# Optimization experiments

Hardware: AMD Instinct MI355X
Metric: run time of the kernel (lower is better)

Reference implementation:

```python
import jax, jax.numpy as jnp
import numpy as np

N_NODES = 50000
N_EDGES = 800000
IN_DIM = 64
HID = 128
OUT_DIM = 64
T_HIST = 8


def setup_inputs() -> dict:
    key = jax.random.key(0)
    ks = jax.random.split(key, 12)
    s = 0.05
    return {
        "node_feats": jax.random.normal(ks[0], (N_NODES, IN_DIM), jnp.float32),
        "history_feats": jax.random.normal(ks[1], (N_NODES, T_HIST, HID), jnp.float32),
        "src": jax.random.randint(ks[2], (N_EDGES,), 0, N_NODES, jnp.int32),
        "dst": jax.random.randint(ks[3], (N_EDGES,), 0, N_NODES, jnp.int32),
        # SAGEConv params (fc_self, fc_neigh share bias as in DGL)
        "W_self": jax.random.normal(ks[4], (IN_DIM, HID), jnp.float32) * s,
        "W_neigh": jax.random.normal(ks[5], (IN_DIM, HID), jnp.float32) * s,
        "b_sage": jnp.zeros((HID,), jnp.float32),
        # LSTM params, PyTorch gate order [i, f, g, o]
        "w_ih": jax.random.normal(ks[6], (HID, 4 * HID), jnp.float32) * s,
        "w_hh": jax.random.normal(ks[7], (HID, 4 * HID), jnp.float32) * s,
        "b_lstm": jnp.zeros((4 * HID,), jnp.float32),
        # classifier
        "W_cls": jax.random.normal(ks[8], (HID, OUT_DIM), jnp.float32) * s,
        "b_cls": jnp.zeros((OUT_DIM,), jnp.float32),
    }


def _lstm_last(x, w_ih, w_hh, b):
    # x: [N, T, H] -> last hidden state [N, H]
    N, T, H = x.shape

    def step(carry, xt):
        h, c = carry
        gates = xt @ w_ih + h @ w_hh + b  # [N, 4H]
        i, f, g, o = jnp.split(gates, 4, axis=-1)
        c = jax.nn.sigmoid(f) * c + jax.nn.sigmoid(i) * jnp.tanh(g)
        h = jax.nn.sigmoid(o) * jnp.tanh(c)
        return (h, c), None

    h0 = jnp.zeros((N, H), x.dtype)
    (h, _), _ = jax.lax.scan(step, (h0, h0), jnp.swapaxes(x, 0, 1))
    return h


def reference(node_feats, history_feats, src, dst, W_self, W_neigh, b_sage,
              w_ih, w_hh, b_lstm, W_cls, b_cls):
    N = node_feats.shape[0]
    # SAGEConv mean aggregation: mean of in-neighbor features per dst node
    msg_sum = jax.ops.segment_sum(node_feats[src], dst, num_segments=N)
    deg = jax.ops.segment_sum(jnp.ones((src.shape[0],), node_feats.dtype),
                              dst, num_segments=N)
    h_neigh = msg_sum / jnp.maximum(deg, 1.0)[:, None]
    h_struct = node_feats @ W_self + h_neigh @ W_neigh + b_sage  # [N, HID]
    # LSTM over history, take last timestep
    h_temp = _lstm_last(history_feats, w_ih, w_hh, b_lstm)  # [N, HID]
    h_combined = h_struct + h_temp
    return h_combined @ W_cls + b_cls  # [N, OUT_DIM]
```

## Files before the change

kernel.cpp:

```cpp
#include <hip/hip_runtime.h>
#include <hip/hip_bf16.h>
#include <stdint.h>

#define N_NODES 50000
#define N_EDGES 800000
#define IN_DIM 64
#define HID 128
#define OUT_DIM 64
#define T_HIST 8

#define NB_SCAN ((N_NODES + 1023) / 1024)

typedef __attribute__((ext_vector_type(8))) short short8;
typedef __attribute__((ext_vector_type(4))) float f32x4;

__device__ __forceinline__ unsigned short f2bf(float x) {
  unsigned int u = __builtin_bit_cast(unsigned int, x);
  unsigned int r = (u + 0x7FFFu + ((u >> 16) & 1u)) >> 16;
  return (unsigned short)r;
}
__device__ __forceinline__ short8 cvt8(float4 a, float4 b) {
  unsigned int w0, w1, w2, w3;
  asm("v_cvt_pk_bf16_f32 %0, %1, %2" : "=v"(w0) : "v"(a.x), "v"(a.y));
  asm("v_cvt_pk_bf16_f32 %0, %1, %2" : "=v"(w1) : "v"(a.z), "v"(a.w));
  asm("v_cvt_pk_bf16_f32 %0, %1, %2" : "=v"(w2) : "v"(b.x), "v"(b.y));
  asm("v_cvt_pk_bf16_f32 %0, %1, %2" : "=v"(w3) : "v"(b.z), "v"(b.w));
  struct { unsigned int a, b, c, d; } s{w0, w1, w2, w3};
  return __builtin_bit_cast(short8, s);
}
__device__ __forceinline__ float sigm(float x) {
  float e = __builtin_amdgcn_exp2f(-1.4426950408889634f * x);
  return __builtin_amdgcn_rcpf(1.f + e);
}
__device__ __forceinline__ float tanh_f(float x) {
  float e = __builtin_amdgcn_exp2f(2.8853900817779268f * x);
  return 1.f - 2.f * __builtin_amdgcn_rcpf(e + 1.f);
}

__global__ void pc_kernel(const float* __restrict__ w_ih, const float* __restrict__ w_hh,
                          const float* __restrict__ W_cls,
                          const float* __restrict__ W_self, const float* __restrict__ W_neigh,
                          const float* __restrict__ b_sage, const float* __restrict__ b_cls,
                          const int* __restrict__ dst,
                          unsigned short* __restrict__ Wt2, unsigned short* __restrict__ Wc2,
                          float* __restrict__ Wsc, float* __restrict__ Wnc,
                          float* __restrict__ bc1, int* __restrict__ cnt) {
  int tid = blockIdx.x * blockDim.x + threadIdx.x;
  int stride = gridDim.x * blockDim.x;
  for (int e = tid; e < N_EDGES; e += stride) atomicAdd(&cnt[dst[e]], 1);
  for (int idx = tid; idx < 256 * 512; idx += stride) {
    int i = idx & 7;
    int lane = (idx >> 3) & 63;
    int F = idx >> 9;
    int q = F >> 5, g = (F >> 3) & 3, kk = F & 7;
    int c = g * 128 + q * 16 + (lane & 15);
    int k = kk * 32 + (lane >> 4) * 8 + i;
    float v = (k < 128) ? w_ih[k * 512 + c] : w_hh[(k - 128) * 512 + c];
    Wt2[idx] = f2bf(v);
  }
  for (int idx = tid; idx < 16 * 512; idx += stride) {
    int i = idx & 7;
    int lane = (idx >> 3) & 63;
    int F = idx >> 9;
    int cb = F >> 2, kk = F & 3;
    int col = cb * 16 + (lane & 15);
    int k = kk * 32 + (lane >> 4) * 8 + i;
    Wc2[idx] = f2bf(W_cls[k * 64 + col]);
  }
  for (int idx = tid; idx < 64 * 64; idx += stride) {
    int k = idx >> 6, c = idx & 63;
    float as = 0.f, an = 0.f;
    for (int m = 0; m < 128; m++) {
      float wc = W_cls[m * 64 + c];
      as += W_self[k * 128 + m] * wc;
      an += W_neigh[k * 128 + m] * wc;
    }
    Wsc[idx] = as;
    Wnc[idx] = an;
  }
  for (int c = tid; c < 64; c += stride) {
    float acc = b_cls[c];
    for (int m = 0; m < 128; m++) acc += b_sage[m] * W_cls[m * 64 + c];
    bc1[c] = acc;
  }
}

__global__ __launch_bounds__(256) void scan1_kernel(const int* __restrict__ cnt,
                                                    int* __restrict__ lexcl, int* __restrict__ btot) {
  __shared__ int sh[256];
  int tid = threadIdx.x;
  int base = blockIdx.x * 1024 + tid * 4;
  int v[4];
  #pragma unroll
  for (int q = 0; q < 4; q++) {
    int i = base + q;
    v[q] = (i < N_NODES) ? cnt[i] : 0;
  }
  int tsum = v[0] + v[1] + v[2] + v[3];
  sh[tid] = tsum;
  __syncthreads();
  int val = tsum;
  for (int off = 1; off < 256; off <<= 1) {
    int x = (tid >= off) ? sh[tid - off] : 0;
    __syncthreads();
    val += x;
    sh[tid] = val;
    __syncthreads();
  }
  int ex = val - tsum;
  if (tid == 255) btot[blockIdx.x] = val;
  #pragma unroll
  for (int q = 0; q < 4; q++) {
    int i = base + q;
    if (i < N_NODES) lexcl[i] = ex;
    ex += v[q];
  }
}

__global__ __launch_bounds__(1024) void scan3_kernel(const int* __restrict__ lexcl,
                                                     const int* __restrict__ btot,
                                                     int* __restrict__ rowstart, int* __restrict__ cursor) {
  int b = blockIdx.x;
  int bs = 0;
  for (int j = 0; j < b; j++) bs += btot[j];
  int i = b * 1024 + threadIdx.x;
  if (i < N_NODES) {
    int rs = lexcl[i] + bs;
    rowstart[i] = rs;
    cursor[i] = rs;
  }
}

__global__ void fill_kernel(const int* __restrict__ src, const int* __restrict__ dst,
                            int* __restrict__ cursor, int* __restrict__ esrc) {
  int e = blockIdx.x * blockDim.x + threadIdx.x;
  if (e < N_EDGES) {
    int d = dst[e];
    int pos = atomicAdd(&cursor[d], 1);
    esrc[pos] = src[e];
  }
}

#define HS_TILE 32
__global__ __launch_bounds__(512) void hstruct_kernel(
    const float* __restrict__ nf, const int* __restrict__ esrc,
    const int* __restrict__ rowstart, const int* __restrict__ cnt,
    const float* __restrict__ Wsc, const float* __restrict__ Wnc, const float* __restrict__ bc1,
    float* __restrict__ out1) {
  __shared__ float s_nf[HS_TILE][IN_DIM + 1];
  __shared__ float s_hn[HS_TILE][IN_DIM + 1];
  int tid = threadIdx.x;
  int node0 = blockIdx.x * HS_TILE;
  for (int i = tid; i < HS_TILE * IN_DIM; i += 512) {
    int r = i >> 6, k = i & 63;
    int node = node0 + r;
    s_nf[r][k] = (node < N_NODES) ? nf[node * 64 + k] : 0.f;
  }
  int wv = tid >> 6, lane = tid & 63;
  for (int r = wv; r < HS_TILE; r += 8) {
    int node = node0 + r;
    float a0 = 0.f, a1 = 0.f, a2 = 0.f, a3 = 0.f;
    int n = 0;
    if (node < N_NODES) {
      n = cnt[node];
      int st = rowstart[node];
      int j = 0;
      for (; j + 4 <= n; j += 4) {
        int s0 = esrc[st + j], s1 = esrc[st + j + 1];
        int s2 = esrc[st + j + 2], s3 = esrc[st + j + 3];
        a0 += nf[s0 * 64 + lane];
        a1 += nf[s1 * 64 + lane];
        a2 += nf[s2 * 64 + lane];
        a3 += nf[s3 * 64 + lane];
      }
      for (; j < n; j++) a0 += nf[esrc[st + j] * 64 + lane];
    }
    s_hn[r][lane] = (a0 + a1 + a2 + a3) * __builtin_amdgcn_rcpf(fmaxf((float)n, 1.f));
  }
  __syncthreads();
  int r = tid & 31;
  int c0 = (tid >> 5) * 4;
  float accs[4] = {0.f, 0.f, 0.f, 0.f};
  for (int k = 0; k < IN_DIM; k++) {
    float a = s_nf[r][k];
    float b = s_hn[r][k];
    float4 w1 = *(const float4*)&Wsc[k * 64 + c0];
    float4 w2 = *(const float4*)&Wnc[k * 64 + c0];
    accs[0] += a * w1.x + b * w2.x;
    accs[1] += a * w1.y + b * w2.y;
    accs[2] += a * w1.z + b * w2.z;
    accs[3] += a * w1.w + b * w2.w;
  }
  int node = node0 + r;
  if (node < N_NODES) {
    #pragma unroll
    for (int i = 0; i < 4; i++)
      out1[(size_t)node * 64 + c0 + i] = accs[i] + bc1[c0 + i];
  }
}

#define LB 32
__global__ __launch_bounds__(512, 2) void lstm_kernel(
    const float* __restrict__ hist,
    const unsigned short* __restrict__ Wt2,
    const unsigned short* __restrict__ Wc2,
    const float* __restrict__ b_lstm,
    const float* __restrict__ out1,
    float* __restrict__ out)
{
  __shared__ alignas(16) unsigned short Abuf[2][LB * 256];

  const int tid = threadIdx.x;
  const int lane = tid & 63;
  const int w = tid >> 6;
  const int l15 = lane & 15;
  const int l4 = lane >> 4;
  const int base = blockIdx.x * LB;
  const int jj = w * 16 + l15;

  short8 Bfr[4][8];
  #pragma unroll
  for (int g = 0; g < 4; g++)
    #pragma unroll
    for (int kk = 0; kk < 8; kk++)
      Bfr[g][kk] = *(const short8*)&Wt2[((w * 32 + g * 8 + kk) * 64 + lane) * 8];

  const float bi  = b_lstm[jj];
  const float bf_ = b_lstm[128 + jj];
  const float bg  = b_lstm[256 + jj];
  const float bo  = b_lstm[384 + jj];

  float c_st[8];
  #pragma unroll
  for (int i = 0; i < 8; i++) c_st[i] = 0.f;

  {
    int row = tid >> 4;
    int kb = tid & 15;
    short8 z = {0,0,0,0,0,0,0,0};
    *(short8*)&Abuf[0][row * 256 + 128 + kb * 8] = z;
    int node = base + row;
    float4 x0 = make_float4(0.f,0.f,0.f,0.f), x1 = make_float4(0.f,0.f,0.f,0.f);
    if (node < N_NODES) {
      const float4* p = (const float4*)&hist[(size_t)node * (T_HIST * HID) + kb * 8];
      x0 = p[0]; x1 = p[1];
    }
    int sb = (kb & 8) | ((kb & 7) ^ (row & 7));
    *(short8*)&Abuf[0][row * 256 + sb * 8] = cvt8(x0, x1);
  }
  __syncthreads();

  float4 xpa, xpb;
  const int srow = tid >> 4, skb = tid & 15;

  #pragma unroll
  for (int t = 0; t < T_HIST - 1; t++) {
    unsigned short* Acur = &Abuf[t & 1][0];
    unsigned short* Anxt = &Abuf[(t & 1) ^ 1][0];

    {
      int node = base + srow;
      if (node < N_NODES) {
        const float4* p = (const float4*)&hist[(size_t)node * (T_HIST * HID) + (t + 1) * HID + skb * 8];
        xpa = p[0]; xpb = p[1];
      } else {
        xpa = make_float4(0.f,0.f,0.f,0.f);
        xpb = make_float4(0.f,0.f,0.f,0.f);
      }
    }

    #pragma unroll
    for (int rb = 0; rb < 2; rb++) {
      f32x4 acc[4];
      #pragma unroll
      for (int g = 0; g < 4; g++) { f32x4 z = {0.f,0.f,0.f,0.f}; acc[g] = z; }
      #pragma unroll
      for (int kk = 0; kk < 8; kk++) {
        int row = rb * 16 + l15;
        int kb = kk * 4 + l4;
        int sb = (kb & 24) | ((kb & 7) ^ (row & 7));
        short8 a = *(const short8*)&Acur[row * 256 + sb * 8];
        #pragma unroll
        for (int g = 0; g < 4; g++)
          acc[g] = __builtin_amdgcn_mfma_f32_16x16x32_bf16(a, Bfr[g][kk], acc[g], 0, 0, 0);
      }
      #pragma unroll
      for (int reg = 0; reg < 4; reg++) {
        int r = rb * 4 + reg;
        float gi = sigm(acc[0][reg] + bi);
        float gf = sigm(acc[1][reg] + bf_);
        float gg = tanh_f(acc[2][reg] + bg);
        float go = sigm(acc[3][reg] + bo);
        float c = gf * c_st[r] + gi * gg;
        c_st[r] = c;
        float h = go * tanh_f(c);
        int row = rb * 16 + l4 * 4 + reg;
        int kb = 16 + (jj >> 3);
        int sb = (kb & 24) | ((kb & 7) ^ (row & 7));
        Anxt[row * 256 + sb * 8 + (jj & 7)] = f2bf(h);
      }
    }

    {
      int sb = (skb & 8) | ((skb & 7) ^ (srow & 7));
      *(short8*)&Anxt[srow * 256 + sb * 8] = cvt8(xpa, xpb);
    }
    __syncthreads();
  }

  {
    unsigned short* Acur = &Abuf[1][0];
    unsigned short* Anxt = &Abuf[0][0];

    #pragma unroll
    for (int rb = 0; rb < 2; rb++) {
      f32x4 acc[4];
      #pragma unroll
      for (int g = 0; g < 4; g++) { f32x4 z = {0.f,0.f,0.f,0.f}; acc[g] = z; }
      #pragma unroll
      for (int kk = 0; kk < 8; kk++) {
        int row = rb * 16 + l15;
        int kb = kk * 4 + l4;
        int sb = (kb & 24) | ((kb & 7) ^ (row & 7));
        short8 a = *(const short8*)&Acur[row * 256 + sb * 8];
        #pragma unroll
        for (int g = 0; g < 4; g++)
          acc[g] = __builtin_amdgcn_mfma_f32_16x16x32_bf16(a, Bfr[g][kk], acc[g], 0, 0, 0);
      }
      #pragma unroll
      for (int reg = 0; reg < 4; reg++) {
        int r = rb * 4 + reg;
        float gi = sigm(acc[0][reg] + bi);
        float gf = sigm(acc[1][reg] + bf_);
        float gg = tanh_f(acc[2][reg] + bg);
        float go = sigm(acc[3][reg] + bo);
        float c = gf * c_st[r] + gi * gg;
        float h = go * tanh_f(c);
        int row = rb * 16 + l4 * 4 + reg;
        int kb = jj >> 3;
        int sb = (kb & 8) | ((kb & 7) ^ (row & 7));
        Anxt[row * 256 + sb * 8 + (jj & 7)] = f2bf(h);
      }
    }
    __syncthreads();

    {
      int rbo = w >> 2, cbo = w & 3;
      int col = cbo * 16 + l15;
      float ov[4];
      #pragma unroll
      for (int reg = 0; reg < 4; reg++) {
        int row = rbo * 16 + l4 * 4 + reg;
        int node = base + row;
        ov[reg] = (node < N_NODES) ? out1[(size_t)node * OUT_DIM + col] : 0.f;
      }
      f32x4 o = {0.f, 0.f, 0.f, 0.f};
      #pragma unroll
      for (int kk = 0; kk < 4; kk++) {
        short8 bv = *(const short8*)&Wc2[((cbo * 4 + kk) * 64 + lane) * 8];
        int row = rbo * 16 + l15;
        int kb = kk * 4 + l4;
        int sb = (kb & 8) | ((kb & 7) ^ (row & 7));
        short8 a = *(const short8*)&Anxt[row * 256 + sb * 8];
        o = __builtin_amdgcn_mfma_f32_16x16x32_bf16(a, bv, o, 0, 0, 0);
      }
      #pragma unroll
      for (int reg = 0; reg < 4; reg++) {
        int row = rbo * 16 + l4 * 4 + reg;
        int node = base + row;
        if (node < N_NODES) out[(size_t)node * OUT_DIM + col] = o[reg] + ov[reg];
      }
    }
  }
}

extern "C" void kernel_launch(void* const* d_in, const int* in_sizes, int n_in,
                              void* d_out, int out_size, void* d_ws, size_t ws_size,
                              hipStream_t stream) {
  (void)in_sizes; (void)n_in; (void)out_size; (void)ws_size;
  const float* node_feats = (const float*)d_in[0];
  const float* hist       = (const float*)d_in[1];
  const int*   src        = (const int*)d_in[2];
  const int*   dst        = (const int*)d_in[3];
  const float* W_self     = (const float*)d_in[4];
  const float* W_neigh    = (const float*)d_in[5];
  const float* b_sage     = (const float*)d_in[6];
  const float* w_ih       = (const float*)d_in[7];
  const float* w_hh       = (const float*)d_in[8];
  const float* b_lstm     = (const float*)d_in[9];
  const float* W_cls      = (const float*)d_in[10];
  const float* b_cls      = (const float*)d_in[11];
  float* out = (float*)d_out;

  char* ws = (char*)d_ws;
  int* cnt        = (int*)(ws);
  int* lexcl      = (int*)(ws + 200192);
  int* rowstart   = (int*)(ws + 400384);
  int* cursor     = (int*)(ws + 600576);
  int* btot       = (int*)(ws + 800768);
  int* esrc       = (int*)(ws + 801792);
  float* out1     = (float*)(ws + 4001792);
  unsigned short* Wt2 = (unsigned short*)(ws + 16801792);
  unsigned short* Wc2 = (unsigned short*)(ws + 17063936);
  float* Wsc      = (float*)(ws + 17080320);
  float* Wnc      = (float*)(ws + 17096704);
  float* bc1      = (float*)(ws + 17113088);

  hipMemsetAsync(cnt, 0, 200000, stream);
  pc_kernel<<<1024, 256, 0, stream>>>(w_ih, w_hh, W_cls, W_self, W_neigh, b_sage, b_cls,
                                      dst, Wt2, Wc2, Wsc, Wnc, bc1, cnt);
  scan1_kernel<<<NB_SCAN, 256, 0, stream>>>(cnt, lexcl, btot);
  scan3_kernel<<<NB_SCAN, 1024, 0, stream>>>(lexcl, btot, rowstart, cursor);
  fill_kernel<<<(N_EDGES + 255) / 256, 256, 0, stream>>>(src, dst, cursor, esrc);
  hstruct_kernel<<<(N_NODES + HS_TILE - 1) / HS_TILE, 512, 0, stream>>>(
      node_feats, esrc, rowstart, cnt, Wsc, Wnc, bc1, out1);
  lstm_kernel<<<(N_NODES + LB - 1) / LB, 512, 0, stream>>>(
      hist, Wt2, Wc2, b_lstm, out1, out);
}
```

Baseline: 357.8 us.

## Merge scan passes, vectorize edge atomics, and interleave neighbor gathers per wave

Fuses the two-pass prefix scan into one kernel. Each block publishes its total through a flagged global slot and spins on earlier blocks' totals, which removes a launch and an intermediate array. Edge counting and CSR fill now read dst/src as int4 to cut load instructions. The neighbor aggregation now processes four nodes per wave at once with wave-uniform counts, so more independent gathers are in flight. The spin-wait relies on all 49 blocks being co-resident, and btot is zeroed by extending the memset.

```diff
diff --git a/kernel.cpp b/kernel.cpp
--- a/kernel.cpp
+++ b/kernel.cpp
@@ -9,7 +9,7 @@
 #define OUT_DIM 64
 #define T_HIST 8
 
-#define NB_SCAN ((N_NODES + 1023) / 1024)
+#define NB_SCAN 49
 
 typedef __attribute__((ext_vector_type(8))) short short8;
 typedef __attribute__((ext_vector_type(4))) float f32x4;
@@ -47,7 +47,14 @@
                           float* __restrict__ bc1, int* __restrict__ cnt) {
   int tid = blockIdx.x * blockDim.x + threadIdx.x;
   int stride = gridDim.x * blockDim.x;
-  for (int e = tid; e < N_EDGES; e += stride) atomicAdd(&cnt[dst[e]], 1);
+  const int4* dst4 = (const int4*)dst;
+  for (int e4 = tid; e4 < N_EDGES / 4; e4 += stride) {
+    int4 d = dst4[e4];
+    atomicAdd(&cnt[d.x], 1);
+    atomicAdd(&cnt[d.y], 1);
+    atomicAdd(&cnt[d.z], 1);
+    atomicAdd(&cnt[d.w], 1);
+  }
   for (int idx = tid; idx < 256 * 512; idx += stride) {
     int i = idx & 7;
     int lane = (idx >> 3) & 63;
@@ -85,47 +92,47 @@
   }
 }
 
-__global__ __launch_bounds__(256) void scan1_kernel(const int* __restrict__ cnt,
-                                                    int* __restrict__ lexcl, int* __restrict__ btot) {
-  __shared__ int sh[256];
+__global__ __launch_bounds__(1024) void scan_kernel(const int* __restrict__ cnt,
+                                                    int* __restrict__ btot,
+                                                    int* __restrict__ rowstart,
+                                                    int* __restrict__ cursor) {
+  __shared__ int sh[1024];
+  __shared__ int s_bs;
   int tid = threadIdx.x;
-  int base = blockIdx.x * 1024 + tid * 4;
-  int v[4];
-  #pragma unroll
-  for (int q = 0; q < 4; q++) {
-    int i = base + q;
-    v[q] = (i < N_NODES) ? cnt[i] : 0;
-  }
-  int tsum = v[0] + v[1] + v[2] + v[3];
-  sh[tid] = tsum;
+  int b = blockIdx.x;
+  int i = b * 1024 + tid;
+  int v = (i < N_NODES) ? cnt[i] : 0;
+  sh[tid] = v;
   __syncthreads();
-  int val = tsum;
-  for (int off = 1; off < 256; off <<= 1) {
+  int val = v;
+  for (int off = 1; off < 1024; off <<= 1) {
     int x = (tid >= off) ? sh[tid - off] : 0;
     __syncthreads();
     val += x;
     sh[tid] = val;
     __syncthreads();
   }
-  int ex = val - tsum;
-  if (tid == 255) btot[blockIdx.x] = val;
-  #pragma unroll
-  for (int q = 0; q < 4; q++) {
-    int i = base + q;
-    if (i < N_NODES) lexcl[i] = ex;
-    ex += v[q];
-  }
-}
-
-__global__ __launch_bounds__(1024) void scan3_kernel(const int* __restrict__ lexcl,
-                                                     const int* __restrict__ btot,
-                                                     int* __restrict__ rowstart, int* __restrict__ cursor) {
-  int b = blockIdx.x;
-  int bs = 0;
-  for (int j = 0; j < b; j++) bs += btot[j];
-  int i = b * 1024 + threadIdx.x;
+  int lex = val - v;
+  if (tid == 1023) atomicExch(&btot[b], val + 1);
+  int contrib = 0;
+  if (tid < b) {
+    int x;
+    do {
+      x = atomicAdd(&btot[tid], 0);
+      if (x == 0) __builtin_amdgcn_s_sleep(2);
+    } while (x == 0);
+    contrib = x - 1;
+  }
+  sh[tid] = contrib;
+  __syncthreads();
+  if (tid == 0) {
+    int bs = 0;
+    for (int j = 0; j < NB_SCAN - 1; j++) bs += sh[j];
+    s_bs = bs;
+  }
+  __syncthreads();
   if (i < N_NODES) {
-    int rs = lexcl[i] + bs;
+    int rs = lex + s_bs;
     rowstart[i] = rs;
     cursor[i] = rs;
   }
@@ -133,11 +140,14 @@
 
 __global__ void fill_kernel(const int* __restrict__ src, const int* __restrict__ dst,
                             int* __restrict__ cursor, int* __restrict__ esrc) {
-  int e = blockIdx.x * blockDim.x + threadIdx.x;
-  if (e < N_EDGES) {
-    int d = dst[e];
-    int pos = atomicAdd(&cursor[d], 1);
-    esrc[pos] = src[e];
+  int e4 = blockIdx.x * blockDim.x + threadIdx.x;
+  if (e4 < N_EDGES / 4) {
+    int4 d = ((const int4*)dst)[e4];
+    int4 s = ((const int4*)src)[e4];
+    esrc[atomicAdd(&cursor[d.x], 1)] = s.x;
+    esrc[atomicAdd(&cursor[d.y], 1)] = s.y;
+    esrc[atomicAdd(&cursor[d.z], 1)] = s.z;
+    esrc[atomicAdd(&cursor[d.w], 1)] = s.w;
   }
 }
 
@@ -157,26 +167,27 @@
     s_nf[r][k] = (node < N_NODES) ? nf[node * 64 + k] : 0.f;
   }
   int wv = tid >> 6, lane = tid & 63;
-  for (int r = wv; r < HS_TILE; r += 8) {
-    int node = node0 + r;
-    float a0 = 0.f, a1 = 0.f, a2 = 0.f, a3 = 0.f;
-    int n = 0;
-    if (node < N_NODES) {
-      n = cnt[node];
-      int st = rowstart[node];
-      int j = 0;
-      for (; j + 4 <= n; j += 4) {
-        int s0 = esrc[st + j], s1 = esrc[st + j + 1];
-        int s2 = esrc[st + j + 2], s3 = esrc[st + j + 3];
-        a0 += nf[s0 * 64 + lane];
-        a1 += nf[s1 * 64 + lane];
-        a2 += nf[s2 * 64 + lane];
-        a3 += nf[s3 * 64 + lane];
-      }
-      for (; j < n; j++) a0 += nf[esrc[st + j] * 64 + lane];
-    }
-    s_hn[r][lane] = (a0 + a1 + a2 + a3) * __builtin_amdgcn_rcpf(fmaxf((float)n, 1.f));
-  }
+  int nn[4], st[4];
+  #pragma unroll
+  for (int rr = 0; rr < 4; rr++) {
+    int node = node0 + wv + rr * 8;
+    int n = 0, s = 0;
+    if (node < N_NODES) { n = cnt[node]; s = rowstart[node]; }
+    nn[rr] = __builtin_amdgcn_readfirstlane(n);
+    st[rr] = __builtin_amdgcn_readfirstlane(s);
+  }
+  float pa[4] = {0.f, 0.f, 0.f, 0.f}, pb[4] = {0.f, 0.f, 0.f, 0.f};
+  int mx = max(max(nn[0], nn[1]), max(nn[2], nn[3]));
+  for (int j = 0; j < mx; j += 2) {
+    #pragma unroll
+    for (int rr = 0; rr < 4; rr++) {
+      if (j < nn[rr])     pa[rr] += nf[(size_t)esrc[st[rr] + j] * 64 + lane];
+      if (j + 1 < nn[rr]) pb[rr] += nf[(size_t)esrc[st[rr] + j + 1] * 64 + lane];
+    }
+  }
+  #pragma unroll
+  for (int rr = 0; rr < 4; rr++)
+    s_hn[wv + rr * 8][lane] = (pa[rr] + pb[rr]) * __builtin_amdgcn_rcpf(fmaxf((float)nn[rr], 1.f));
   __syncthreads();
   int r = tid & 31;
   int c0 = (tid >> 5) * 4;
@@ -394,24 +405,22 @@
 
   char* ws = (char*)d_ws;
   int* cnt        = (int*)(ws);
-  int* lexcl      = (int*)(ws + 200192);
-  int* rowstart   = (int*)(ws + 400384);
-  int* cursor     = (int*)(ws + 600576);
-  int* btot       = (int*)(ws + 800768);
-  int* esrc       = (int*)(ws + 801792);
-  float* out1     = (float*)(ws + 4001792);
-  unsigned short* Wt2 = (unsigned short*)(ws + 16801792);
-  unsigned short* Wc2 = (unsigned short*)(ws + 17063936);
-  float* Wsc      = (float*)(ws + 17080320);
-  float* Wnc      = (float*)(ws + 17096704);
-  float* bc1      = (float*)(ws + 17113088);
-
-  hipMemsetAsync(cnt, 0, 200000, stream);
+  int* btot       = (int*)(ws + 200192);
+  int* rowstart   = (int*)(ws + 200448);
+  int* cursor     = (int*)(ws + 400640);
+  int* esrc       = (int*)(ws + 600832);
+  float* out1     = (float*)(ws + 3800832);
+  unsigned short* Wt2 = (unsigned short*)(ws + 16600832);
+  unsigned short* Wc2 = (unsigned short*)(ws + 16862976);
+  float* Wsc      = (float*)(ws + 16879360);
+  float* Wnc      = (float*)(ws + 16895744);
+  float* bc1      = (float*)(ws + 16912128);
+
+  hipMemsetAsync(cnt, 0, 200448, stream);
   pc_kernel<<<1024, 256, 0, stream>>>(w_ih, w_hh, W_cls, W_self, W_neigh, b_sage, b_cls,
                                       dst, Wt2, Wc2, Wsc, Wnc, bc1, cnt);
-  scan1_kernel<<<NB_SCAN, 256, 0, stream>>>(cnt, lexcl, btot);
-  scan3_kernel<<<NB_SCAN, 1024, 0, stream>>>(lexcl, btot, rowstart, cursor);
-  fill_kernel<<<(N_EDGES + 255) / 256, 256, 0, stream>>>(src, dst, cursor, esrc);
+  scan_kernel<<<NB_SCAN, 1024, 0, stream>>>(cnt, btot, rowstart, cursor);
+  fill_kernel<<<(N_EDGES / 4 + 255) / 256, 256, 0, stream>>>(src, dst, cursor, esrc);
   hstruct_kernel<<<(N_NODES + HS_TILE - 1) / HS_TILE, 512, 0, stream>>>(
       node_feats, esrc, rowstart, cnt, Wsc, Wnc, bc1, out1);
   lstm_kernel<<<(N_NODES + LB - 1) / LB, 512, 0, stream>>>(
```

Measured after the change: 389.0 us. +8.7%, slower.
